# Performance work log

Measured on AMD Instinct MI355X. Metric: run time of the kernel, lower is better.

Reference implementation:

```python
import jax, jax.numpy as jnp
import numpy as np

N, E, B = 16384, 65536, 32
D_IN, ED, H, L = 4, 5, 64, 3  # node feat, edge feat, hidden=output, num layers
NEG_SLOPE = 0.1
EPS = 1e-5


def _leaky(v):
    return jnp.where(v > 0, v, NEG_SLOPE * v)


def setup_inputs() -> dict:
    key = jax.random.key(0)
    ks = jax.random.split(key, 32)
    s = 0.05
    inp = {
        'x': jax.random.normal(ks[0], (N, D_IN), jnp.float32),
        'edge_index': jax.random.randint(ks[1], (2, E), 0, N),
        'edge_attr': jax.random.normal(ks[2], (E, ED), jnp.float32),
        'batch': jnp.sort(jax.random.randint(ks[3], (N,), 0, B)),
        # input projection Linear(4 -> H)
        'W_in': s * jax.random.normal(ks[4], (H, D_IN), jnp.float32),
        'b_in': jnp.zeros((H,), jnp.float32),
        # per-layer edge MLP: Linear(ED->H), Linear(H->H), Linear(H->H*H); stacked over L
        'ew1': s * jax.random.normal(ks[5], (L, H, ED), jnp.float32),
        'eb1': jnp.zeros((L, H), jnp.float32),
        'ew2': s * jax.random.normal(ks[6], (L, H, H), jnp.float32),
        'eb2': jnp.zeros((L, H), jnp.float32),
        'ew3': s * jax.random.normal(ks[7], (L, H * H, H), jnp.float32),
        'eb3': jnp.zeros((L, H * H), jnp.float32),
        # NNConv root weight + bias per layer
        'root_w': s * jax.random.normal(ks[8], (L, H, H), jnp.float32),
        'root_b': jnp.zeros((L, H), jnp.float32),
        # LayerNorm per layer
        'ln_g': jnp.ones((L, H), jnp.float32),
        'ln_b': jnp.zeros((L, H), jnp.float32),
        # prediction head: Linear(H->H), Linear(H->H//2), Linear(H//2->1)
        'pw1': s * jax.random.normal(ks[9], (H, H), jnp.float32),
        'pb1': jnp.zeros((H,), jnp.float32),
        'pw2': s * jax.random.normal(ks[10], (H // 2, H), jnp.float32),
        'pb2': jnp.zeros((H // 2,), jnp.float32),
        'pw3': s * jax.random.normal(ks[11], (1, H // 2), jnp.float32),
        'pb3': jnp.zeros((1,), jnp.float32),
    }
    return inp


def reference(x, edge_index, edge_attr, batch, W_in, b_in, ew1, eb1, ew2, eb2,
              ew3, eb3, root_w, root_b, ln_g, ln_b, pw1, pb1, pw2, pb2, pw3, pb3):
    src, dst = edge_index[0], edge_index[1]
    n_nodes = x.shape[0]
    n_edges = edge_attr.shape[0]
    # in-degree for scatter-mean (PyG yields 0 for isolated nodes)
    deg = jax.ops.segment_sum(jnp.ones((n_edges,), x.dtype), dst, num_segments=n_nodes)
    deg = jnp.maximum(deg, 1.0)[:, None]

    # input projection (dropout = identity in eval)
    h = _leaky(x @ W_in.T + b_in)

    for l in range(L):
        # edge MLP -> per-edge weight matrix [E, H, H]
        e = _leaky(edge_attr @ ew1[l].T + eb1[l])
        e = _leaky(e @ ew2[l].T + eb2[l])
        Wf = (e @ ew3[l].T + eb3[l]).reshape(n_edges, H, H)
        # message = x_src @ W_edge, scatter-mean to dst
        msg = jnp.einsum('ei,eio->eo', h[src], Wf)
        agg = jax.ops.segment_sum(msg, dst, num_segments=n_nodes) / deg
        out = agg + h @ root_w[l].T + root_b[l]
        # LayerNorm (post-norm)
        mu = out.mean(-1, keepdims=True)
        var = ((out - mu) ** 2).mean(-1, keepdims=True)
        out = (out - mu) * jax.lax.rsqrt(var + EPS) * ln_g[l] + ln_b[l]
        # activation + (identity) dropout + residual (in==out for all layers)
        h = _leaky(out) + h

    # global mean pool over graphs
    pooled = jax.ops.segment_sum(h, batch, num_segments=B)
    cnt = jax.ops.segment_sum(jnp.ones((n_nodes,), h.dtype), batch, num_segments=B)
    pooled = pooled / jnp.maximum(cnt, 1.0)[:, None]

    # prediction head
    p = _leaky(pooled @ pw1.T + pb1)
    p = _leaky(p @ pw2.T + pb2)
    pred = (p @ pw3.T + pb3).squeeze(-1)  # [B]
    return pred
```

## Files before the change

kernel.cpp:

```cpp
#include <hip/hip_runtime.h>
#include <hip/hip_bf16.h>

#define N_NODES 16384
#define N_EDGES 65536
#define NB      32
#define H       64
#define NLAYERS 3
#define NEG     0.1f
#define LN_EPS  1e-5f

typedef _Float16 f16;
typedef _Float16 f16x2 __attribute__((ext_vector_type(2)));
typedef _Float16 f16x8 __attribute__((ext_vector_type(8)));
typedef __fp16   hf16x2 __attribute__((ext_vector_type(2)));
typedef float    f32x16 __attribute__((ext_vector_type(16)));

union F16x8 { f16x8 v; f16x2 p[4]; int4 i4; int2 i2[2]; };
union F16x2U { f16x2 h2; hf16x2 raw; unsigned int u; };
union F16U   { f16 h; unsigned short u; };

__device__ __forceinline__ f16x2 pkrtz(float a, float b) {
    F16x2U t; t.raw = __builtin_amdgcn_cvt_pkrtz(a, b); return t.h2;
}
__device__ __forceinline__ float leaky(float v) { return v > 0.f ? v : NEG * v; }

__global__ __launch_bounds__(256) void k_setup(const float* __restrict__ x,
                                               const float* __restrict__ Win,
                                               const float* __restrict__ bin,
                                               const int* __restrict__ dst,
                                               const float* __restrict__ ew3,
                                               const float* __restrict__ eb3,
                                               float* __restrict__ h,
                                               float* __restrict__ deg,
                                               f16* __restrict__ Bp) {
    int bid = blockIdx.x;
    if (bid < 4096) {
        int t = bid * 256 + threadIdx.x;
        int n = t >> 6, j = t & 63;
        const float* xr = x + n * 4;
        const float* wr = Win + j * 4;
        float v = bin[j] + xr[0] * wr[0] + xr[1] * wr[1] + xr[2] * wr[2] + xr[3] * wr[3];
        h[t] = leaky(v);
    } else if (bid < 4352) {
        int e = (bid - 4096) * 256 + threadIdx.x;
        atomicAdd(&deg[dst[e]], 1.0f);
    } else {
        int tg    = (bid - 4352) * 256 + threadIdx.x;
        int lane  = tg & 63;
        int gslot = tg >> 6;
        int l     = gslot / 520;
        int slot  = gslot - l * 520;
        const float* ew3l = ew3 + (size_t)l * 262144;
        const float* eb3l = eb3 + (size_t)l * 4096;
        int i   = slot >> 3;
        int rem = slot & 7;
        int ks  = rem >> 1;
        int oq  = rem & 1;
        int o   = oq * 32 + (lane & 31);
        int k0  = ks * 16 + (lane >> 5) * 8;
        float v[8];
        if (i < 64) {
            const float* s = ew3l + ((size_t)(i * 64 + o)) * 64 + k0;
            float4 a = ((const float4*)s)[0];
            float4 b = ((const float4*)s)[1];
            v[0] = a.x; v[1] = a.y; v[2] = a.z; v[3] = a.w;
            v[4] = b.x; v[5] = b.y; v[6] = b.z; v[7] = b.w;
        } else {
#pragma unroll
            for (int j = 0; j < 8; j++) v[j] = eb3l[(k0 + j) * 64 + o];
        }
        union { int4 i4; f16 a[8]; } out;
#pragma unroll
        for (int j = 0; j < 8; j++) out.a[j] = (f16)v[j];
        *(int4*)(Bp + (size_t)l * 266240 + (size_t)slot * 512 + lane * 8) = out.i4;
    }
}

#define HS_STRIDE 76

__device__ __forceinline__ void loadB8(const f16* __restrict__ Bp, int c, int oq, int lane, F16x8* dstB) {
    const f16* base = Bp + (((size_t)(c * 16 + oq)) << 9) + lane * 8;
#pragma unroll
    for (int di = 0; di < 2; di++)
#pragma unroll
        for (int ks = 0; ks < 4; ks++)
            dstB[di * 4 + ks].i4 = *(const int4*)(base + ((di * 8 + ks * 2) << 9));
}
__device__ __forceinline__ void loadB4(const f16* __restrict__ Bp, int oq, int lane, F16x8* dstB) {
    const f16* base = Bp + (((size_t)(512 + oq)) << 9) + lane * 8;
#pragma unroll
    for (int ks = 0; ks < 4; ks++)
        dstB[ks].i4 = *(const int4*)(base + ((ks * 2) << 9));
}

__device__ __forceinline__ void msg_chunk2(int c, const F16x8* __restrict__ B,
                                           const unsigned short* hp0,
                                           const unsigned short* hp1,
                                           const f16x2 (*e2p)[4][4], f32x16* CC) {
    unsigned int rr0 = *(const unsigned int*)(hp0 + 2 * c);
    unsigned int rr1 = *(const unsigned int*)(hp1 + 2 * c);
    F16x2U h00, h01, h10, h11;
    h00.u = __builtin_amdgcn_perm(rr0, rr0, 0x01000100u);
    h10.u = __builtin_amdgcn_perm(rr0, rr0, 0x03020302u);
    h01.u = __builtin_amdgcn_perm(rr1, rr1, 0x01000100u);
    h11.u = __builtin_amdgcn_perm(rr1, rr1, 0x03020302u);
#pragma unroll
    for (int ks = 0; ks < 4; ks++) {
        F16x8 A00, A01, A10, A11;
#pragma unroll
        for (int r = 0; r < 4; r++) {
            A00.p[r] = h00.h2 * e2p[0][ks][r];
            A01.p[r] = h01.h2 * e2p[1][ks][r];
            A10.p[r] = h10.h2 * e2p[0][ks][r];
            A11.p[r] = h11.h2 * e2p[1][ks][r];
        }
        CC[0] = __builtin_amdgcn_mfma_f32_32x32x16_f16(A00.v, B[0 * 4 + ks].v, CC[0], 0, 0, 0);
        CC[1] = __builtin_amdgcn_mfma_f32_32x32x16_f16(A01.v, B[0 * 4 + ks].v, CC[1], 0, 0, 0);
        CC[2] = __builtin_amdgcn_mfma_f32_32x32x16_f16(A10.v, B[1 * 4 + ks].v, CC[2], 0, 0, 0);
        CC[3] = __builtin_amdgcn_mfma_f32_32x32x16_f16(A11.v, B[1 * 4 + ks].v, CC[3], 0, 0, 0);
    }
}

__global__ __launch_bounds__(256, 2) void k_msg(const float* __restrict__ h,
                                                const float* __restrict__ ea,
                                                const float* __restrict__ w1,
                                                const float* __restrict__ b1,
                                                const float* __restrict__ w2,
                                                const float* __restrict__ b2,
                                                const f16* __restrict__ Bp,
                                                const int* __restrict__ src,
                                                const int* __restrict__ dst,
                                                float* __restrict__ agg) {
    __shared__ __align__(16) unsigned short hsL[128 * HS_STRIDE];
    __shared__ __align__(16) unsigned short e1L[128 * 72];
    __shared__ __align__(16) unsigned short e2L[128 * 72];
    __shared__ float eas[128 * 8];
    __shared__ int dstL[128];

    const int t    = threadIdx.x;
    const int lane = t & 63;
    const int w    = t >> 6;
    const int eh   = w >> 1, oq = w & 1;
    const int m    = lane & 31;
    const int kp   = lane >> 5;
    const int eb   = blockIdx.x * 128;

    for (int idx = t; idx < 640; idx += 256) {
        int r = idx / 5, d = idx - r * 5;
        eas[r * 8 + d] = ea[(size_t)eb * 5 + idx];
    }
    {
        int e    = t >> 1;
        int half = t & 1;
        int nsrc = src[eb + e];
        const float4* hr = (const float4*)(h + (size_t)nsrc * 64 + half * 32);
        unsigned int* hrow = (unsigned int*)hsL + e * (HS_STRIDE / 2) + half * 16;
#pragma unroll
        for (int q = 0; q < 8; q++) {
            float4 v = hr[q];
            F16x2U p0, p1;
            p0.raw = __builtin_amdgcn_cvt_pkrtz(v.x, v.y);
            p1.raw = __builtin_amdgcn_cvt_pkrtz(v.z, v.w);
            hrow[q * 2 + 0] = p0.u;
            hrow[q * 2 + 1] = p1.u;
        }
        if (t < 128) dstL[t] = dst[eb + t];
    }
    __syncthreads();

    {
        int kk = t & 63;
        int eg = t >> 6;
        float w1r[5];
#pragma unroll
        for (int d = 0; d < 5; d++) w1r[d] = w1[kk * 5 + d];
        float b1r = b1[kk];
#pragma unroll 4
        for (int g = 0; g < 32; g++) {
            int row = eg * 32 + g;
            float4 a4 = *(const float4*)(eas + row * 8);
            float a5 = eas[row * 8 + 4];
            float v = b1r + a4.x * w1r[0] + a4.y * w1r[1] + a4.z * w1r[2] + a4.w * w1r[3] + a5 * w1r[4];
            F16U z; z.h = (f16)leaky(v);
            e1L[row * 72 + kk] = z.u;
        }
    }
    __syncthreads();

    {
        F16x8 W2f[4];
#pragma unroll
        for (int ks = 0; ks < 4; ks++) {
            const float* s = w2 + (size_t)(oq * 32 + m) * 64 + ks * 16 + kp * 8;
            float4 a = ((const float4*)s)[0];
            float4 b = ((const float4*)s)[1];
            W2f[ks].p[0] = pkrtz(a.x, a.y);
            W2f[ks].p[1] = pkrtz(a.z, a.w);
            W2f[ks].p[2] = pkrtz(b.x, b.y);
            W2f[ks].p[3] = pkrtz(b.z, b.w);
        }
        float b2r = b2[oq * 32 + m];
#pragma unroll
        for (int tt = 0; tt < 2; tt++) {
            f32x16 C2 = {0,0,0,0,0,0,0,0,0,0,0,0,0,0,0,0};
#pragma unroll
            for (int ks = 0; ks < 4; ks++) {
                F16x8 A;
                A.i4 = *(const int4*)(e1L + (size_t)((eh * 2 + tt) * 32 + m) * 72 + ks * 16 + kp * 8);
                C2 = __builtin_amdgcn_mfma_f32_32x32x16_f16(A.v, W2f[ks].v, C2, 0, 0, 0);
            }
#pragma unroll
            for (int reg = 0; reg < 16; reg++) {
                int r = (reg & 3) + 8 * (reg >> 2) + 4 * kp;
                F16U z; z.h = (f16)leaky(C2[reg] + b2r);
                e2L[((eh * 2 + tt) * 32 + r) * 72 + oq * 32 + m] = z.u;
            }
        }
    }
    __syncthreads();

    f16x2 e2p[2][4][4];
#pragma unroll
    for (int tt = 0; tt < 2; tt++) {
#pragma unroll
        for (int ks = 0; ks < 4; ks++) {
            F16x8 q;
            q.i4 = *(const int4*)(e2L + (size_t)((eh * 2 + tt) * 32 + m) * 72 + ks * 16 + kp * 8);
            e2p[tt][ks][0] = q.p[0]; e2p[tt][ks][1] = q.p[1];
            e2p[tt][ks][2] = q.p[2]; e2p[tt][ks][3] = q.p[3];
        }
    }

    f32x16 CC[4];
#pragma unroll
    for (int q = 0; q < 4; q++)
#pragma unroll
        for (int r = 0; r < 16; r++) CC[q][r] = 0.f;

    const unsigned short* hp0 = hsL + ((eh * 2 + 0) * 32 + m) * HS_STRIDE;
    const unsigned short* hp1 = hsL + ((eh * 2 + 1) * 32 + m) * HS_STRIDE;

    F16x8 B0[8], B1[8];
    loadB8(Bp, 0, oq, lane, B0);
    loadB8(Bp, 1, oq, lane, B1);
    for (int it = 0; it < 15; it++) {
        int c = it * 2;
        msg_chunk2(c,     B0, hp0, hp1, e2p, CC);  loadB8(Bp, c + 2, oq, lane, B0);
        msg_chunk2(c + 1, B1, hp0, hp1, e2p, CC);  loadB8(Bp, c + 3, oq, lane, B1);
    }
    msg_chunk2(30, B0, hp0, hp1, e2p, CC);
    loadB4(Bp, oq, lane, B0);
    msg_chunk2(31, B1, hp0, hp1, e2p, CC);

#pragma unroll
    for (int ks = 0; ks < 4; ks++) {
        int koff = (ks * 16 + kp * 8) * 2;
        const char* r0p = (const char*)hsL + (size_t)((eh * 2 + 0) * 32 + m) * (HS_STRIDE * 2) + koff;
        const char* r1p = (const char*)hsL + (size_t)((eh * 2 + 1) * 32 + m) * (HS_STRIDE * 2) + koff;
        F16x8 A0, A1;
        A0.i2[0] = *(const int2*)(r0p); A0.i2[1] = *(const int2*)(r0p + 8);
        A1.i2[0] = *(const int2*)(r1p); A1.i2[1] = *(const int2*)(r1p + 8);
        CC[0] = __builtin_amdgcn_mfma_f32_32x32x16_f16(A0.v, B0[ks].v, CC[0], 0, 0, 0);
        CC[1] = __builtin_amdgcn_mfma_f32_32x32x16_f16(A1.v, B0[ks].v, CC[1], 0, 0, 0);
    }

    int o = oq * 32 + m;
#pragma unroll
    for (int reg = 0; reg < 16; reg++) {
        int r = (reg & 3) + 8 * (reg >> 2) + 4 * kp;
        atomicAdd(&agg[(size_t)dstL[(eh * 2 + 0) * 32 + r] * 64 + o], CC[0][reg] + CC[2][reg]);
    }
#pragma unroll
    for (int reg = 0; reg < 16; reg++) {
        int r = (reg & 3) + 8 * (reg >> 2) + 4 * kp;
        atomicAdd(&agg[(size_t)dstL[(eh * 2 + 1) * 32 + r] * 64 + o], CC[1][reg] + CC[3][reg]);
    }
}

__global__ __launch_bounds__(256) void k_node(const float* __restrict__ agg,
                                              const float* __restrict__ deg,
                                              const float* __restrict__ rw,
                                              const float* __restrict__ rb,
                                              const float* __restrict__ lg,
                                              const float* __restrict__ lb,
                                              float* __restrict__ h,
                                              const int* __restrict__ batch,
                                              float* __restrict__ pooled,
                                              int last) {
    __shared__ __align__(16) unsigned short hA[64 * 72];
    __shared__ float outL[64][68];
    int t = threadIdx.x;
    int nb = blockIdx.x * 64;
    int lane = t & 63, w = t >> 6;
    int nq = w >> 1, oq = w & 1;
    int m = lane & 31, kp = lane >> 5;

    {
        int r = t >> 2, c0 = (t & 3) * 16;
        const float4* hr = (const float4*)(h + (size_t)(nb + r) * 64 + c0);
        unsigned int* drow = (unsigned int*)hA + r * 36 + c0 / 2;
#pragma unroll
        for (int q = 0; q < 4; q++) {
            float4 v = hr[q];
            F16x2U p0, p1;
            p0.raw = __builtin_amdgcn_cvt_pkrtz(v.x, v.y);
            p1.raw = __builtin_amdgcn_cvt_pkrtz(v.z, v.w);
            drow[q * 2] = p0.u; drow[q * 2 + 1] = p1.u;
        }
    }
    F16x8 Bf[4];
#pragma unroll
    for (int ks = 0; ks < 4; ks++) {
        const float* s = rw + (size_t)(oq * 32 + m) * 64 + ks * 16 + kp * 8;
        float4 a = ((const float4*)s)[0];
        float4 b = ((const float4*)s)[1];
        Bf[ks].p[0] = pkrtz(a.x, a.y);
        Bf[ks].p[1] = pkrtz(a.z, a.w);
        Bf[ks].p[2] = pkrtz(b.x, b.y);
        Bf[ks].p[3] = pkrtz(b.z, b.w);
    }
    __syncthreads();

    f32x16 C = {0,0,0,0,0,0,0,0,0,0,0,0,0,0,0,0};
#pragma unroll
    for (int ks = 0; ks < 4; ks++) {
        F16x8 A;
        A.i4 = *(const int4*)(hA + (size_t)(nq * 32 + m) * 72 + ks * 16 + kp * 8);
        C = __builtin_amdgcn_mfma_f32_32x32x16_f16(A.v, Bf[ks].v, C, 0, 0, 0);
    }

    int o = oq * 32 + m;
#pragma unroll
    for (int reg = 0; reg < 16; reg++) {
        int r = (reg & 3) + 8 * (reg >> 2) + 4 * kp;
        int n = nq * 32 + r;
        outL[n][o] = C[reg] + rb[o] + agg[(size_t)(nb + n) * 64 + o] / fmaxf(deg[nb + n], 1.0f);
    }
    __syncthreads();

    float gj = lg[lane], bj = lb[lane];
    float accp = 0.f;
    int cur = batch[nb + w * 16];
    for (int q = 0; q < 16; q++) {
        int n = w * 16 + q;
        float v = outL[n][lane];
        float mu = v;
#pragma unroll
        for (int msk = 32; msk > 0; msk >>= 1) mu += __shfl_xor(mu, msk);
        mu *= (1.f / 64.f);
        float d = v - mu;
        float var = d * d;
#pragma unroll
        for (int msk = 32; msk > 0; msk >>= 1) var += __shfl_xor(var, msk);
        var *= (1.f / 64.f);
        float ov = d * rsqrtf(var + LN_EPS) * gj + bj;
        float hn = leaky(ov) + h[(size_t)(nb + n) * 64 + lane];
        h[(size_t)(nb + n) * 64 + lane] = hn;
        if (last) {
            int b = batch[nb + n];
            if (b != cur) { atomicAdd(&pooled[cur * 64 + lane], accp); accp = 0.f; cur = b; }
            accp += hn;
        }
    }
    if (last) atomicAdd(&pooled[cur * 64 + lane], accp);
}

__global__ __launch_bounds__(256) void k_head(const float* __restrict__ pooled,
                                              const int* __restrict__ batch,
                                              const float* __restrict__ pw1, const float* __restrict__ pb1,
                                              const float* __restrict__ pw2, const float* __restrict__ pb2,
                                              const float* __restrict__ pw3, const float* __restrict__ pb3,
                                              float* __restrict__ out) {
    __shared__ float cntL[32];
    __shared__ float ps[32][64];
    __shared__ float p1[32][64];
    __shared__ float p2[32][32];
    int t = threadIdx.x;
    if (t < 32) cntL[t] = 0.f;
    __syncthreads();
    {
        const int4* bp4 = (const int4*)(batch + t * 64);
        int cur = batch[t * 64];
        float c = 0.f;
        for (int q = 0; q < 16; q++) {
            int4 b4 = bp4[q];
            int bs[4] = { b4.x, b4.y, b4.z, b4.w };
#pragma unroll
            for (int e = 0; e < 4; e++) {
                if (bs[e] != cur) { atomicAdd(&cntL[cur], c); cur = bs[e]; c = 0.f; }
                c += 1.f;
            }
        }
        atomicAdd(&cntL[cur], c);
    }
    __syncthreads();
    for (int idx = t; idx < 2048; idx += 256) {
        int b = idx >> 6, j = idx & 63;
        ps[b][j] = pooled[idx] / fmaxf(cntL[b], 1.0f);
    }
    __syncthreads();
    for (int idx = t; idx < 2048; idx += 256) {
        int b = idx >> 6, j = idx & 63;
        float v = pb1[j];
#pragma unroll 8
        for (int i = 0; i < 64; i++) v += ps[b][i] * pw1[j * 64 + i];
        p1[b][j] = leaky(v);
    }
    __syncthreads();
    for (int idx = t; idx < 1024; idx += 256) {
        int b = idx >> 5, j = idx & 31;
        float v = pb2[j];
#pragma unroll 8
        for (int i = 0; i < 64; i++) v += p1[b][i] * pw2[j * 64 + i];
        p2[b][j] = leaky(v);
    }
    __syncthreads();
    if (t < 32) {
        float v = pb3[0];
#pragma unroll 8
        for (int i = 0; i < 32; i++) v += p2[t][i] * pw3[i];
        out[t] = v;
    }
}

extern "C" void kernel_launch(void* const* d_in, const int* in_sizes, int n_in,
                              void* d_out, int out_size, void* d_ws, size_t ws_size,
                              hipStream_t stream) {
    const float* x    = (const float*)d_in[0];
    const int*   eidx = (const int*)  d_in[1];
    const float* ea   = (const float*)d_in[2];
    const int*   bat  = (const int*)  d_in[3];
    const float* Win  = (const float*)d_in[4];
    const float* bin  = (const float*)d_in[5];
    const float* ew1  = (const float*)d_in[6];
    const float* eb1  = (const float*)d_in[7];
    const float* ew2  = (const float*)d_in[8];
    const float* eb2  = (const float*)d_in[9];
    const float* ew3  = (const float*)d_in[10];
    const float* eb3  = (const float*)d_in[11];
    const float* rw   = (const float*)d_in[12];
    const float* rb   = (const float*)d_in[13];
    const float* lg   = (const float*)d_in[14];
    const float* lb   = (const float*)d_in[15];
    const float* pw1  = (const float*)d_in[16];
    const float* pb1  = (const float*)d_in[17];
    const float* pw2  = (const float*)d_in[18];
    const float* pb2  = (const float*)d_in[19];
    const float* pw3  = (const float*)d_in[20];
    const float* pb3  = (const float*)d_in[21];
    float* out = (float*)d_out;

    float* ws     = (float*)d_ws;
    float* h      = ws;
    float* agg    = ws + 1048576;
    float* deg    = ws + 4194304;
    float* pooled = ws + 4210688;
    f16*   Bp     = (f16*)(ws + 4212800);

    const int* srcp = eidx;
    const int* dstp = eidx + N_EDGES;

    (void)hipMemsetAsync(agg, 0, (size_t)3164224 * sizeof(float), stream);

    k_setup<<<4742, 256, 0, stream>>>(x, Win, bin, dstp, ew3, eb3, h, deg, Bp);

    for (int l = 0; l < NLAYERS; l++) {
        float* agg_l = agg + (size_t)l * N_NODES * H;
        k_msg <<<N_EDGES / 128, 256, 0, stream>>>(h, ea, ew1 + l * 320, eb1 + l * 64,
                                                  ew2 + l * 4096, eb2 + l * 64,
                                                  Bp + (size_t)l * 266240,
                                                  srcp, dstp, agg_l);
        k_node<<<N_NODES / 64, 256, 0, stream>>>(agg_l, deg, rw + l * 4096, rb + l * 64,
                                                 lg + l * 64, lb + l * 64, h,
                                                 bat, pooled, l == NLAYERS - 1 ? 1 : 0);
    }

    k_head<<<1, 256, 0, stream>>>(pooled, bat, pw1, pb1, pw2, pb2, pw3, pb3, out);
}
```

Baseline: 325.6 us.

## Fuse all stages into one persistent cooperative kernel with grid syncs

Replaces the memset, setup, per-layer message/node kernels and head with a single cooperative launch of 256 blocks that uses grid.sync between stages. Each block processes two edge tiles per layer and one node tile, and shared memory is unioned across stages. The aim is to remove the roughly nine kernel launch gaps and the separate memset. In exchange it runs at one block per CU with 256 blocks, so occupancy and latency hiding during the heavy message phase may be lower than with the previous 512-block, two-blocks-per-CU launch. It falls back to the multi-kernel path if the cooperative launch fails.

```diff
diff --git a/kernel.cpp b/kernel.cpp
--- a/kernel.cpp
+++ b/kernel.cpp
@@ -1,5 +1,8 @@
 #include <hip/hip_runtime.h>
+#include <hip/hip_cooperative_groups.h>
 #include <hip/hip_bf16.h>
+
+namespace cg = cooperative_groups;
 
 #define N_NODES 16384
 #define N_EDGES 65536
@@ -8,6 +11,7 @@
 #define NLAYERS 3
 #define NEG     0.1f
 #define LN_EPS  1e-5f
+#define HS_STRIDE 76
 
 typedef _Float16 f16;
 typedef _Float16 f16x2 __attribute__((ext_vector_type(2)));
@@ -23,6 +27,444 @@
     F16x2U t; t.raw = __builtin_amdgcn_cvt_pkrtz(a, b); return t.h2;
 }
 __device__ __forceinline__ float leaky(float v) { return v > 0.f ? v : NEG * v; }
+
+struct Params {
+    const float* x; const int* eidx; const float* ea; const int* bat;
+    const float* Win; const float* bin;
+    const float* ew1; const float* eb1; const float* ew2; const float* eb2;
+    const float* ew3; const float* eb3;
+    const float* rw;  const float* rb;  const float* lg;  const float* lb;
+    const float* pw1; const float* pb1; const float* pw2; const float* pb2;
+    const float* pw3; const float* pb3;
+    float* out; float* ws;
+};
+
+struct MsgSmem {
+    unsigned short hsL[128 * HS_STRIDE];
+    unsigned short e1L[128 * 72];
+    unsigned short e2L[128 * 72];
+    float eas[128 * 8];
+    int dstL[128];
+};
+struct NodeSmem {
+    unsigned short hA[64 * 72];
+    float outL[64][68];
+};
+struct HeadSmem {
+    float cntL[32];
+    float ps[32][64];
+    float p1[32][64];
+    float p2[32][32];
+};
+union __align__(16) AllSmem { MsgSmem m; NodeSmem n; HeadSmem hd; };
+
+__device__ __forceinline__ void loadB8(const f16* __restrict__ Bp, int c, int oq, int lane, F16x8* dstB) {
+    const f16* base = Bp + (((size_t)(c * 16 + oq)) << 9) + lane * 8;
+#pragma unroll
+    for (int di = 0; di < 2; di++)
+#pragma unroll
+        for (int ks = 0; ks < 4; ks++)
+            dstB[di * 4 + ks].i4 = *(const int4*)(base + ((di * 8 + ks * 2) << 9));
+}
+__device__ __forceinline__ void loadB4(const f16* __restrict__ Bp, int oq, int lane, F16x8* dstB) {
+    const f16* base = Bp + (((size_t)(512 + oq)) << 9) + lane * 8;
+#pragma unroll
+    for (int ks = 0; ks < 4; ks++)
+        dstB[ks].i4 = *(const int4*)(base + ((ks * 2) << 9));
+}
+
+__device__ __forceinline__ void msg_chunk2(int c, const F16x8* __restrict__ B,
+                                           const unsigned short* hp0,
+                                           const unsigned short* hp1,
+                                           const f16x2 (*e2p)[4][4], f32x16* CC) {
+    unsigned int rr0 = *(const unsigned int*)(hp0 + 2 * c);
+    unsigned int rr1 = *(const unsigned int*)(hp1 + 2 * c);
+    F16x2U h00, h01, h10, h11;
+    h00.u = __builtin_amdgcn_perm(rr0, rr0, 0x01000100u);
+    h10.u = __builtin_amdgcn_perm(rr0, rr0, 0x03020302u);
+    h01.u = __builtin_amdgcn_perm(rr1, rr1, 0x01000100u);
+    h11.u = __builtin_amdgcn_perm(rr1, rr1, 0x03020302u);
+#pragma unroll
+    for (int ks = 0; ks < 4; ks++) {
+        F16x8 A00, A01, A10, A11;
+#pragma unroll
+        for (int r = 0; r < 4; r++) {
+            A00.p[r] = h00.h2 * e2p[0][ks][r];
+            A01.p[r] = h01.h2 * e2p[1][ks][r];
+            A10.p[r] = h10.h2 * e2p[0][ks][r];
+            A11.p[r] = h11.h2 * e2p[1][ks][r];
+        }
+        CC[0] = __builtin_amdgcn_mfma_f32_32x32x16_f16(A00.v, B[0 * 4 + ks].v, CC[0], 0, 0, 0);
+        CC[1] = __builtin_amdgcn_mfma_f32_32x32x16_f16(A01.v, B[0 * 4 + ks].v, CC[1], 0, 0, 0);
+        CC[2] = __builtin_amdgcn_mfma_f32_32x32x16_f16(A10.v, B[1 * 4 + ks].v, CC[2], 0, 0, 0);
+        CC[3] = __builtin_amdgcn_mfma_f32_32x32x16_f16(A11.v, B[1 * 4 + ks].v, CC[3], 0, 0, 0);
+    }
+}
+
+__device__ __forceinline__ void msg_body(MsgSmem& S, const float* __restrict__ h,
+        const float* __restrict__ ea,
+        const float* __restrict__ w1, const float* __restrict__ b1,
+        const float* __restrict__ w2, const float* __restrict__ b2,
+        const f16* __restrict__ Bpl,
+        const int* __restrict__ srcp, const int* __restrict__ dstp,
+        float* __restrict__ agg_l, int eb, int t) {
+    const int lane = t & 63;
+    const int w    = t >> 6;
+    const int eh   = w >> 1, oq = w & 1;
+    const int m    = lane & 31;
+    const int kp   = lane >> 5;
+
+    for (int idx = t; idx < 640; idx += 256) {
+        int r = idx / 5, d = idx - r * 5;
+        S.eas[r * 8 + d] = ea[(size_t)eb * 5 + idx];
+    }
+    {
+        int e    = t >> 1;
+        int half = t & 1;
+        int nsrc = srcp[eb + e];
+        const float4* hr = (const float4*)(h + (size_t)nsrc * 64 + half * 32);
+        unsigned int* hrow = (unsigned int*)S.hsL + e * (HS_STRIDE / 2) + half * 16;
+#pragma unroll
+        for (int q = 0; q < 8; q++) {
+            float4 v = hr[q];
+            F16x2U p0, p1;
+            p0.raw = __builtin_amdgcn_cvt_pkrtz(v.x, v.y);
+            p1.raw = __builtin_amdgcn_cvt_pkrtz(v.z, v.w);
+            hrow[q * 2 + 0] = p0.u;
+            hrow[q * 2 + 1] = p1.u;
+        }
+        if (t < 128) S.dstL[t] = dstp[eb + t];
+    }
+    __syncthreads();
+
+    {
+        int kk = t & 63;
+        int eg = t >> 6;
+        float w1r[5];
+#pragma unroll
+        for (int d = 0; d < 5; d++) w1r[d] = w1[kk * 5 + d];
+        float b1r = b1[kk];
+#pragma unroll 4
+        for (int g = 0; g < 32; g++) {
+            int row = eg * 32 + g;
+            float4 a4 = *(const float4*)(S.eas + row * 8);
+            float a5 = S.eas[row * 8 + 4];
+            float v = b1r + a4.x * w1r[0] + a4.y * w1r[1] + a4.z * w1r[2] + a4.w * w1r[3] + a5 * w1r[4];
+            F16U z; z.h = (f16)leaky(v);
+            S.e1L[row * 72 + kk] = z.u;
+        }
+    }
+    __syncthreads();
+
+    {
+        F16x8 W2f[4];
+#pragma unroll
+        for (int ks = 0; ks < 4; ks++) {
+            const float* s = w2 + (size_t)(oq * 32 + m) * 64 + ks * 16 + kp * 8;
+            float4 a = ((const float4*)s)[0];
+            float4 b = ((const float4*)s)[1];
+            W2f[ks].p[0] = pkrtz(a.x, a.y);
+            W2f[ks].p[1] = pkrtz(a.z, a.w);
+            W2f[ks].p[2] = pkrtz(b.x, b.y);
+            W2f[ks].p[3] = pkrtz(b.z, b.w);
+        }
+        float b2r = b2[oq * 32 + m];
+#pragma unroll
+        for (int tt = 0; tt < 2; tt++) {
+            f32x16 C2 = {0,0,0,0,0,0,0,0,0,0,0,0,0,0,0,0};
+#pragma unroll
+            for (int ks = 0; ks < 4; ks++) {
+                F16x8 A;
+                A.i4 = *(const int4*)(S.e1L + (size_t)((eh * 2 + tt) * 32 + m) * 72 + ks * 16 + kp * 8);
+                C2 = __builtin_amdgcn_mfma_f32_32x32x16_f16(A.v, W2f[ks].v, C2, 0, 0, 0);
+            }
+#pragma unroll
+            for (int reg = 0; reg < 16; reg++) {
+                int r = (reg & 3) + 8 * (reg >> 2) + 4 * kp;
+                F16U z; z.h = (f16)leaky(C2[reg] + b2r);
+                S.e2L[((eh * 2 + tt) * 32 + r) * 72 + oq * 32 + m] = z.u;
+            }
+        }
+    }
+    __syncthreads();
+
+    f16x2 e2p[2][4][4];
+#pragma unroll
+    for (int tt = 0; tt < 2; tt++) {
+#pragma unroll
+        for (int ks = 0; ks < 4; ks++) {
+            F16x8 q;
+            q.i4 = *(const int4*)(S.e2L + (size_t)((eh * 2 + tt) * 32 + m) * 72 + ks * 16 + kp * 8);
+            e2p[tt][ks][0] = q.p[0]; e2p[tt][ks][1] = q.p[1];
+            e2p[tt][ks][2] = q.p[2]; e2p[tt][ks][3] = q.p[3];
+        }
+    }
+
+    f32x16 CC[4];
+#pragma unroll
+    for (int q = 0; q < 4; q++)
+#pragma unroll
+        for (int r = 0; r < 16; r++) CC[q][r] = 0.f;
+
+    const unsigned short* hp0 = S.hsL + ((eh * 2 + 0) * 32 + m) * HS_STRIDE;
+    const unsigned short* hp1 = S.hsL + ((eh * 2 + 1) * 32 + m) * HS_STRIDE;
+
+    F16x8 B0[8], B1[8];
+    loadB8(Bpl, 0, oq, lane, B0);
+    loadB8(Bpl, 1, oq, lane, B1);
+    for (int it = 0; it < 15; it++) {
+        int c = it * 2;
+        msg_chunk2(c,     B0, hp0, hp1, e2p, CC);  loadB8(Bpl, c + 2, oq, lane, B0);
+        msg_chunk2(c + 1, B1, hp0, hp1, e2p, CC);  loadB8(Bpl, c + 3, oq, lane, B1);
+    }
+    msg_chunk2(30, B0, hp0, hp1, e2p, CC);
+    loadB4(Bpl, oq, lane, B0);
+    msg_chunk2(31, B1, hp0, hp1, e2p, CC);
+#pragma unroll
+    for (int ks = 0; ks < 4; ks++) {
+        int koff = (ks * 16 + kp * 8) * 2;
+        const char* r0p = (const char*)S.hsL + (size_t)((eh * 2 + 0) * 32 + m) * (HS_STRIDE * 2) + koff;
+        const char* r1p = (const char*)S.hsL + (size_t)((eh * 2 + 1) * 32 + m) * (HS_STRIDE * 2) + koff;
+        F16x8 A0, A1;
+        A0.i2[0] = *(const int2*)(r0p); A0.i2[1] = *(const int2*)(r0p + 8);
+        A1.i2[0] = *(const int2*)(r1p); A1.i2[1] = *(const int2*)(r1p + 8);
+        CC[0] = __builtin_amdgcn_mfma_f32_32x32x16_f16(A0.v, B0[ks].v, CC[0], 0, 0, 0);
+        CC[1] = __builtin_amdgcn_mfma_f32_32x32x16_f16(A1.v, B0[ks].v, CC[1], 0, 0, 0);
+    }
+
+    int o = oq * 32 + m;
+#pragma unroll
+    for (int reg = 0; reg < 16; reg++) {
+        int r = (reg & 3) + 8 * (reg >> 2) + 4 * kp;
+        atomicAdd(&agg_l[(size_t)S.dstL[(eh * 2 + 0) * 32 + r] * 64 + o], CC[0][reg] + CC[2][reg]);
+    }
+#pragma unroll
+    for (int reg = 0; reg < 16; reg++) {
+        int r = (reg & 3) + 8 * (reg >> 2) + 4 * kp;
+        atomicAdd(&agg_l[(size_t)S.dstL[(eh * 2 + 1) * 32 + r] * 64 + o], CC[1][reg] + CC[3][reg]);
+    }
+}
+
+__device__ __forceinline__ void node_body(NodeSmem& S, float* __restrict__ h,
+        const float* __restrict__ agg_l, const float* __restrict__ deg,
+        const float* __restrict__ rwl, const float* __restrict__ rbl,
+        const float* __restrict__ lgl, const float* __restrict__ lbl,
+        const int* __restrict__ bat, float* __restrict__ pooled,
+        int last, int nb, int t) {
+    const int lane = t & 63, w = t >> 6;
+    const int nq = w >> 1, oq = w & 1;
+    const int m = lane & 31, kp = lane >> 5;
+
+    {
+        int r = t >> 2, c0 = (t & 3) * 16;
+        const float4* hr = (const float4*)(h + (size_t)(nb + r) * 64 + c0);
+        unsigned int* drow = (unsigned int*)S.hA + r * 36 + c0 / 2;
+#pragma unroll
+        for (int q = 0; q < 4; q++) {
+            float4 v = hr[q];
+            F16x2U p0, p1;
+            p0.raw = __builtin_amdgcn_cvt_pkrtz(v.x, v.y);
+            p1.raw = __builtin_amdgcn_cvt_pkrtz(v.z, v.w);
+            drow[q * 2] = p0.u; drow[q * 2 + 1] = p1.u;
+        }
+    }
+    F16x8 Bf[4];
+#pragma unroll
+    for (int ks = 0; ks < 4; ks++) {
+        const float* s = rwl + (size_t)(oq * 32 + m) * 64 + ks * 16 + kp * 8;
+        float4 a = ((const float4*)s)[0];
+        float4 b = ((const float4*)s)[1];
+        Bf[ks].p[0] = pkrtz(a.x, a.y);
+        Bf[ks].p[1] = pkrtz(a.z, a.w);
+        Bf[ks].p[2] = pkrtz(b.x, b.y);
+        Bf[ks].p[3] = pkrtz(b.z, b.w);
+    }
+    __syncthreads();
+
+    f32x16 C = {0,0,0,0,0,0,0,0,0,0,0,0,0,0,0,0};
+#pragma unroll
+    for (int ks = 0; ks < 4; ks++) {
+        F16x8 A;
+        A.i4 = *(const int4*)(S.hA + (size_t)(nq * 32 + m) * 72 + ks * 16 + kp * 8);
+        C = __builtin_amdgcn_mfma_f32_32x32x16_f16(A.v, Bf[ks].v, C, 0, 0, 0);
+    }
+
+    int o = oq * 32 + m;
+#pragma unroll
+    for (int reg = 0; reg < 16; reg++) {
+        int r = (reg & 3) + 8 * (reg >> 2) + 4 * kp;
+        int n = nq * 32 + r;
+        S.outL[n][o] = C[reg] + rbl[o] + agg_l[(size_t)(nb + n) * 64 + o] / fmaxf(deg[nb + n], 1.0f);
+    }
+    __syncthreads();
+
+    float gj = lgl[lane], bj = lbl[lane];
+    float accp = 0.f;
+    int cur = bat[nb + w * 16];
+    for (int q = 0; q < 16; q++) {
+        int n = w * 16 + q;
+        float v = S.outL[n][lane];
+        float mu = v;
+#pragma unroll
+        for (int msk = 32; msk > 0; msk >>= 1) mu += __shfl_xor(mu, msk);
+        mu *= (1.f / 64.f);
+        float d = v - mu;
+        float var = d * d;
+#pragma unroll
+        for (int msk = 32; msk > 0; msk >>= 1) var += __shfl_xor(var, msk);
+        var *= (1.f / 64.f);
+        float ov = d * rsqrtf(var + LN_EPS) * gj + bj;
+        float hn = leaky(ov) + h[(size_t)(nb + n) * 64 + lane];
+        h[(size_t)(nb + n) * 64 + lane] = hn;
+        if (last) {
+            int b = bat[nb + n];
+            if (b != cur) { atomicAdd(&pooled[cur * 64 + lane], accp); accp = 0.f; cur = b; }
+            accp += hn;
+        }
+    }
+    if (last) atomicAdd(&pooled[cur * 64 + lane], accp);
+}
+
+__device__ __forceinline__ void head_body(HeadSmem& S, const float* __restrict__ pooled,
+        const int* __restrict__ bat,
+        const float* pw1, const float* pb1, const float* pw2, const float* pb2,
+        const float* pw3, const float* pb3, float* __restrict__ out, int t) {
+    if (t < 32) S.cntL[t] = 0.f;
+    __syncthreads();
+    {
+        const int4* bp4 = (const int4*)(bat + t * 64);
+        int cur = bat[t * 64];
+        float c = 0.f;
+        for (int q = 0; q < 16; q++) {
+            int4 b4 = bp4[q];
+            int bs[4] = { b4.x, b4.y, b4.z, b4.w };
+#pragma unroll
+            for (int e = 0; e < 4; e++) {
+                if (bs[e] != cur) { atomicAdd(&S.cntL[cur], c); cur = bs[e]; c = 0.f; }
+                c += 1.f;
+            }
+        }
+        atomicAdd(&S.cntL[cur], c);
+    }
+    __syncthreads();
+    for (int idx = t; idx < 2048; idx += 256) {
+        int b = idx >> 6, j = idx & 63;
+        S.ps[b][j] = pooled[idx] / fmaxf(S.cntL[b], 1.0f);
+    }
+    __syncthreads();
+    for (int idx = t; idx < 2048; idx += 256) {
+        int b = idx >> 6, j = idx & 63;
+        float v = pb1[j];
+#pragma unroll 8
+        for (int i = 0; i < 64; i++) v += S.ps[b][i] * pw1[j * 64 + i];
+        S.p1[b][j] = leaky(v);
+    }
+    __syncthreads();
+    for (int idx = t; idx < 1024; idx += 256) {
+        int b = idx >> 5, j = idx & 31;
+        float v = pb2[j];
+#pragma unroll 8
+        for (int i = 0; i < 64; i++) v += S.p1[b][i] * pw2[j * 64 + i];
+        S.p2[b][j] = leaky(v);
+    }
+    __syncthreads();
+    if (t < 32) {
+        float v = pb3[0];
+#pragma unroll 8
+        for (int i = 0; i < 32; i++) v += S.p2[t][i] * pw3[i];
+        out[t] = v;
+    }
+}
+
+__global__ __launch_bounds__(256, 1) void k_all(Params P) {
+    __shared__ AllSmem smem;
+    cg::grid_group grid = cg::this_grid();
+
+    const int t    = threadIdx.x;
+    const int bid  = blockIdx.x;
+    const int lane = t & 63;
+    const int w    = t >> 6;
+    const int m    = lane & 31;
+    const int kp   = lane >> 5;
+
+    float* ws     = P.ws;
+    float* h      = ws;
+    float* agg    = ws + 1048576;
+    float* deg    = ws + 4194304;
+    float* pooled = ws + 4210688;
+    f16*   Bp     = (f16*)(ws + 4212800);
+    const int* srcp = P.eidx;
+    const int* dstp = P.eidx + N_EDGES;
+
+    {
+        float4* z = (float4*)(ws + 1048576);
+        for (int i = bid * 256 + t; i < 791056; i += 256 * 256)
+            z[i] = make_float4(0.f, 0.f, 0.f, 0.f);
+    }
+    grid.sync();
+
+    {
+        int base = bid * 4096;
+#pragma unroll
+        for (int q = 0; q < 16; q++) {
+            int idx = base + q * 256 + t;
+            int n = idx >> 6, j = idx & 63;
+            const float* xr = P.x + n * 4;
+            const float* wr = P.Win + j * 4;
+            float v = P.bin[j] + xr[0] * wr[0] + xr[1] * wr[1] + xr[2] * wr[2] + xr[3] * wr[3];
+            h[idx] = leaky(v);
+        }
+        atomicAdd(&deg[dstp[bid * 256 + t]], 1.0f);
+        for (int gslot = bid * 4 + w; gslot < 1560; gslot += 1024) {
+            int l     = gslot / 520;
+            int slot  = gslot - l * 520;
+            const float* ew3l = P.ew3 + (size_t)l * 262144;
+            const float* eb3l = P.eb3 + (size_t)l * 4096;
+            int i   = slot >> 3;
+            int rem = slot & 7;
+            int ks  = rem >> 1;
+            int oq  = rem & 1;
+            int o   = oq * 32 + m;
+            int k0  = ks * 16 + kp * 8;
+            float v[8];
+            if (i < 64) {
+                const float* s = ew3l + ((size_t)(i * 64 + o)) * 64 + k0;
+                float4 a = ((const float4*)s)[0];
+                float4 b = ((const float4*)s)[1];
+                v[0] = a.x; v[1] = a.y; v[2] = a.z; v[3] = a.w;
+                v[4] = b.x; v[5] = b.y; v[6] = b.z; v[7] = b.w;
+            } else {
+#pragma unroll
+                for (int j = 0; j < 8; j++) v[j] = eb3l[(k0 + j) * 64 + o];
+            }
+            union { int4 i4; f16 a[8]; } outw;
+#pragma unroll
+            for (int j = 0; j < 8; j++) outw.a[j] = (f16)v[j];
+            *(int4*)(Bp + (size_t)l * 266240 + (size_t)slot * 512 + lane * 8) = outw.i4;
+        }
+    }
+    grid.sync();
+
+    for (int l = 0; l < NLAYERS; l++) {
+        float* agg_l = agg + (size_t)l * 1048576;
+#pragma unroll 1
+        for (int g = 0; g < 2; g++) {
+            if (g) __syncthreads();
+            msg_body(smem.m, h, P.ea, P.ew1 + l * 320, P.eb1 + l * 64,
+                     P.ew2 + l * 4096, P.eb2 + l * 64,
+                     Bp + (size_t)l * 266240, srcp, dstp, agg_l,
+                     (g * 256 + bid) * 128, t);
+        }
+        grid.sync();
+        node_body(smem.n, h, agg_l, deg, P.rw + l * 4096, P.rb + l * 64,
+                  P.lg + l * 64, P.lb + l * 64, P.bat, pooled,
+                  (l == NLAYERS - 1) ? 1 : 0, bid * 64, t);
+        grid.sync();
+    }
+
+    if (bid == 0)
+        head_body(smem.hd, pooled, P.bat, P.pw1, P.pb1, P.pw2, P.pb2, P.pw3, P.pb3, P.out, t);
+}
 
 __global__ __launch_bounds__(256) void k_setup(const float* __restrict__ x,
                                                const float* __restrict__ Win,
@@ -69,411 +511,105 @@
 #pragma unroll
             for (int j = 0; j < 8; j++) v[j] = eb3l[(k0 + j) * 64 + o];
         }
-        union { int4 i4; f16 a[8]; } out;
-#pragma unroll
-        for (int j = 0; j < 8; j++) out.a[j] = (f16)v[j];
-        *(int4*)(Bp + (size_t)l * 266240 + (size_t)slot * 512 + lane * 8) = out.i4;
-    }
-}
-
-#define HS_STRIDE 76
-
-__device__ __forceinline__ void loadB8(const f16* __restrict__ Bp, int c, int oq, int lane, F16x8* dstB) {
-    const f16* base = Bp + (((size_t)(c * 16 + oq)) << 9) + lane * 8;
-#pragma unroll
-    for (int di = 0; di < 2; di++)
-#pragma unroll
-        for (int ks = 0; ks < 4; ks++)
-            dstB[di * 4 + ks].i4 = *(const int4*)(base + ((di * 8 + ks * 2) << 9));
-}
-__device__ __forceinline__ void loadB4(const f16* __restrict__ Bp, int oq, int lane, F16x8* dstB) {
-    const f16* base = Bp + (((size_t)(512 + oq)) << 9) + lane * 8;
-#pragma unroll
-    for (int ks = 0; ks < 4; ks++)
-        dstB[ks].i4 = *(const int4*)(base + ((ks * 2) << 9));
-}
-
-__device__ __forceinline__ void msg_chunk2(int c, const F16x8* __restrict__ B,
-                                           const unsigned short* hp0,
-                                           const unsigned short* hp1,
-                                           const f16x2 (*e2p)[4][4], f32x16* CC) {
-    unsigned int rr0 = *(const unsigned int*)(hp0 + 2 * c);
-    unsigned int rr1 = *(const unsigned int*)(hp1 + 2 * c);
-    F16x2U h00, h01, h10, h11;
-    h00.u = __builtin_amdgcn_perm(rr0, rr0, 0x01000100u);
-    h10.u = __builtin_amdgcn_perm(rr0, rr0, 0x03020302u);
-    h01.u = __builtin_amdgcn_perm(rr1, rr1, 0x01000100u);
-    h11.u = __builtin_amdgcn_perm(rr1, rr1, 0x03020302u);
-#pragma unroll
-    for (int ks = 0; ks < 4; ks++) {
-        F16x8 A00, A01, A10, A11;
-#pragma unroll
-        for (int r = 0; r < 4; r++) {
-            A00.p[r] = h00.h2 * e2p[0][ks][r];
-            A01.p[r] = h01.h2 * e2p[1][ks][r];
-            A10.p[r] = h10.h2 * e2p[0][ks][r];
-            A11.p[r] = h11.h2 * e2p[1][ks][r];
-        }
-        CC[0] = __builtin_amdgcn_mfma_f32_32x32x16_f16(A00.v, B[0 * 4 + ks].v, CC[0], 0, 0, 0);
-        CC[1] = __builtin_amdgcn_mfma_f32_32x32x16_f16(A01.v, B[0 * 4 + ks].v, CC[1], 0, 0, 0);
-        CC[2] = __builtin_amdgcn_mfma_f32_32x32x16_f16(A10.v, B[1 * 4 + ks].v, CC[2], 0, 0, 0);
-        CC[3] = __builtin_amdgcn_mfma_f32_32x32x16_f16(A11.v, B[1 * 4 + ks].v, CC[3], 0, 0, 0);
-    }
-}
-
-__global__ __launch_bounds__(256, 2) void k_msg(const float* __restrict__ h,
-                                                const float* __restrict__ ea,
-                                                const float* __restrict__ w1,
-                                                const float* __restrict__ b1,
-                                                const float* __restrict__ w2,
-                                                const float* __restrict__ b2,
-                                                const f16* __restrict__ Bp,
-                                                const int* __restrict__ src,
-                                                const int* __restrict__ dst,
-                                                float* __restrict__ agg) {
-    __shared__ __align__(16) unsigned short hsL[128 * HS_STRIDE];
-    __shared__ __align__(16) unsigned short e1L[128 * 72];
-    __shared__ __align__(16) unsigned short e2L[128 * 72];
-    __shared__ float eas[128 * 8];
-    __shared__ int dstL[128];
-
-    const int t    = threadIdx.x;
-    const int lane = t & 63;
-    const int w    = t >> 6;
-    const int eh   = w >> 1, oq = w & 1;
-    const int m    = lane & 31;
-    const int kp   = lane >> 5;
-    const int eb   = blockIdx.x * 128;
-
-    for (int idx = t; idx < 640; idx += 256) {
-        int r = idx / 5, d = idx - r * 5;
-        eas[r * 8 + d] = ea[(size_t)eb * 5 + idx];
-    }
-    {
-        int e    = t >> 1;
-        int half = t & 1;
-        int nsrc = src[eb + e];
-        const float4* hr = (const float4*)(h + (size_t)nsrc * 64 + half * 32);
-        unsigned int* hrow = (unsigned int*)hsL + e * (HS_STRIDE / 2) + half * 16;
-#pragma unroll
-        for (int q = 0; q < 8; q++) {
-            float4 v = hr[q];
-            F16x2U p0, p1;
-            p0.raw = __builtin_amdgcn_cvt_pkrtz(v.x, v.y);
-            p1.raw = __builtin_amdgcn_cvt_pkrtz(v.z, v.w);
-            hrow[q * 2 + 0] = p0.u;
-            hrow[q * 2 + 1] = p1.u;
-        }
-        if (t < 128) dstL[t] = dst[eb + t];
-    }
-    __syncthreads();
-
-    {
-        int kk = t & 63;
-        int eg = t >> 6;
-        float w1r[5];
-#pragma unroll
-        for (int d = 0; d < 5; d++) w1r[d] = w1[kk * 5 + d];
-        float b1r = b1[kk];
-#pragma unroll 4
-        for (int g = 0; g < 32; g++) {
-            int row = eg * 32 + g;
-            float4 a4 = *(const float4*)(eas + row * 8);
-            float a5 = eas[row * 8 + 4];
-            float v = b1r + a4.x * w1r[0] + a4.y * w1r[1] + a4.z * w1r[2] + a4.w * w1r[3] + a5 * w1r[4];
-            F16U z; z.h = (f16)leaky(v);
-            e1L[row * 72 + kk] = z.u;
-        }
-    }
-    __syncthreads();
-
-    {
-        F16x8 W2f[4];
-#pragma unroll
-        for (int ks = 0; ks < 4; ks++) {
-            const float* s = w2 + (size_t)(oq * 32 + m) * 64 + ks * 16 + kp * 8;
-            float4 a = ((const float4*)s)[0];
-            float4 b = ((const float4*)s)[1];
-            W2f[ks].p[0] = pkrtz(a.x, a.y);
-            W2f[ks].p[1] = pkrtz(a.z, a.w);
-            W2f[ks].p[2] = pkrtz(b.x, b.y);
-            W2f[ks].p[3] = pkrtz(b.z, b.w);
-        }
-        float b2r = b2[oq * 32 + m];
-#pragma unroll
-        for (int tt = 0; tt < 2; tt++) {
-            f32x16 C2 = {0,0,0,0,0,0,0,0,0,0,0,0,0,0,0,0};
-#pragma unroll
-            for (int ks = 0; ks < 4; ks++) {
-                F16x8 A;
-                A.i4 = *(const int4*)(e1L + (size_t)((eh * 2 + tt) * 32 + m) * 72 + ks * 16 + kp * 8);
-                C2 = __builtin_amdgcn_mfma_f32_32x32x16_f16(A.v, W2f[ks].v, C2, 0, 0, 0);
-            }
-#pragma unroll
-            for (int reg = 0; reg < 16; reg++) {
-                int r = (reg & 3) + 8 * (reg >> 2) + 4 * kp;
-                F16U z; z.h = (f16)leaky(C2[reg] + b2r);
-                e2L[((eh * 2 + tt) * 32 + r) * 72 + oq * 32 + m] = z.u;
-            }
-        }
-    }
-    __syncthreads();
-
-    f16x2 e2p[2][4][4];
-#pragma unroll
-    for (int tt = 0; tt < 2; tt++) {
-#pragma unroll
-        for (int ks = 0; ks < 4; ks++) {
-            F16x8 q;
-            q.i4 = *(const int4*)(e2L + (size_t)((eh * 2 + tt) * 32 + m) * 72 + ks * 16 + kp * 8);
-            e2p[tt][ks][0] = q.p[0]; e2p[tt][ks][1] = q.p[1];
-            e2p[tt][ks][2] = q.p[2]; e2p[tt][ks][3] = q.p[3];
-        }
-    }
-
-    f32x16 CC[4];
-#pragma unroll
-    for (int q = 0; q < 4; q++)
-#pragma unroll
-        for (int r = 0; r < 16; r++) CC[q][r] = 0.f;
-
-    const unsigned short* hp0 = hsL + ((eh * 2 + 0) * 32 + m) * HS_STRIDE;
-    const unsigned short* hp1 = hsL + ((eh * 2 + 1) * 32 + m) * HS_STRIDE;
-
-    F16x8 B0[8], B1[8];
-    loadB8(Bp, 0, oq, lane, B0);
-    loadB8(Bp, 1, oq, lane, B1);
-    for (int it = 0; it < 15; it++) {
-        int c = it * 2;
-        msg_chunk2(c,     B0, hp0, hp1, e2p, CC);  loadB8(Bp, c + 2, oq, lane, B0);
-        msg_chunk2(c + 1, B1, hp0, hp1, e2p, CC);  loadB8(Bp, c + 3, oq, lane, B1);
-    }
-    msg_chunk2(30, B0, hp0, hp1, e2p, CC);
-    loadB4(Bp, oq, lane, B0);
-    msg_chunk2(31, B1, hp0, hp1, e2p, CC);
-
-#pragma unroll
-    for (int ks = 0; ks < 4; ks++) {
-        int koff = (ks * 16 + kp * 8) * 2;
-        const char* r0p = (const char*)hsL + (size_t)((eh * 2 + 0) * 32 + m) * (HS_STRIDE * 2) + koff;
-        const char* r1p = (const char*)hsL + (size_t)((eh * 2 + 1) * 32 + m) * (HS_STRIDE * 2) + koff;
-        F16x8 A0, A1;
-        A0.i2[0] = *(const int2*)(r0p); A0.i2[1] = *(const int2*)(r0p + 8);
-        A1.i2[0] = *(const int2*)(r1p); A1.i2[1] = *(const int2*)(r1p + 8);
-        CC[0] = __builtin_amdgcn_mfma_f32_32x32x16_f16(A0.v, B0[ks].v, CC[0], 0, 0, 0);
-        CC[1] = __builtin_amdgcn_mfma_f32_32x32x16_f16(A1.v, B0[ks].v, CC[1], 0, 0, 0);
-    }
-
-    int o = oq * 32 + m;
-#pragma unroll
-    for (int reg = 0; reg < 16; reg++) {
-        int r = (reg & 3) + 8 * (reg >> 2) + 4 * kp;
-        atomicAdd(&agg[(size_t)dstL[(eh * 2 + 0) * 32 + r] * 64 + o], CC[0][reg] + CC[2][reg]);
-    }
-#pragma unroll
-    for (int reg = 0; reg < 16; reg++) {
-        int r = (reg & 3) + 8 * (reg >> 2) + 4 * kp;
-        atomicAdd(&agg[(size_t)dstL[(eh * 2 + 1) * 32 + r] * 64 + o], CC[1][reg] + CC[3][reg]);
-    }
-}
-
-__global__ __launch_bounds__(256) void k_node(const float* __restrict__ agg,
-                                              const float* __restrict__ deg,
-                                              const float* __restrict__ rw,
-                                              const float* __restrict__ rb,
-                                              const float* __restrict__ lg,
-                                              const float* __restrict__ lb,
-                                              float* __restrict__ h,
-                                              const int* __restrict__ batch,
-                                              float* __restrict__ pooled,
-                                              int last) {
-    __shared__ __align__(16) unsigned short hA[64 * 72];
-    __shared__ float outL[64][68];
-    int t = threadIdx.x;
-    int nb = blockIdx.x * 64;
-    int lane = t & 63, w = t >> 6;
-    int nq = w >> 1, oq = w & 1;
-    int m = lane & 31, kp = lane >> 5;
-
-    {
-        int r = t >> 2, c0 = (t & 3) * 16;
-        const float4* hr = (const float4*)(h + (size_t)(nb + r) * 64 + c0);
-        unsigned int* drow = (unsigned int*)hA + r * 36 + c0 / 2;
-#pragma unroll
-        for (int q = 0; q < 4; q++) {
-            float4 v = hr[q];
-            F16x2U p0, p1;
-            p0.raw = __builtin_amdgcn_cvt_pkrtz(v.x, v.y);
-            p1.raw = __builtin_amdgcn_cvt_pkrtz(v.z, v.w);
-            drow[q * 2] = p0.u; drow[q * 2 + 1] = p1.u;
-        }
-    }
-    F16x8 Bf[4];
-#pragma unroll
-    for (int ks = 0; ks < 4; ks++) {
-        const float* s = rw + (size_t)(oq * 32 + m) * 64 + ks * 16 + kp * 8;
-        float4 a = ((const float4*)s)[0];
-        float4 b = ((const float4*)s)[1];
-        Bf[ks].p[0] = pkrtz(a.x, a.y);
-        Bf[ks].p[1] = pkrtz(a.z, a.w);
-        Bf[ks].p[2] = pkrtz(b.x, b.y);
-        Bf[ks].p[3] = pkrtz(b.z, b.w);
-    }
-    __syncthreads();
-
-    f32x16 C = {0,0,0,0,0,0,0,0,0,0,0,0,0,0,0,0};
-#pragma unroll
-    for (int ks = 0; ks < 4; ks++) {
-        F16x8 A;
-        A.i4 = *(const int4*)(hA + (size_t)(nq * 32 + m) * 72 + ks * 16 + kp * 8);
-        C = __builtin_amdgcn_mfma_f32_32x32x16_f16(A.v, Bf[ks].v, C, 0, 0, 0);
-    }
-
-    int o = oq * 32 + m;
-#pragma unroll
-    for (int reg = 0; reg < 16; reg++) {
-        int r = (reg & 3) + 8 * (reg >> 2) + 4 * kp;
-        int n = nq * 32 + r;
-        outL[n][o] = C[reg] + rb[o] + agg[(size_t)(nb + n) * 64 + o] / fmaxf(deg[nb + n], 1.0f);
-    }
-    __syncthreads();
-
-    float gj = lg[lane], bj = lb[lane];
-    float accp = 0.f;
-    int cur = batch[nb + w * 16];
-    for (int q = 0; q < 16; q++) {
-        int n = w * 16 + q;
-        float v = outL[n][lane];
-        float mu = v;
-#pragma unroll
-        for (int msk = 32; msk > 0; msk >>= 1) mu += __shfl_xor(mu, msk);
-        mu *= (1.f / 64.f);
-        float d = v - mu;
-        float var = d * d;
-#pragma unroll
-        for (int msk = 32; msk > 0; msk >>= 1) var += __shfl_xor(var, msk);
-        var *= (1.f / 64.f);
-        float ov = d * rsqrtf(var + LN_EPS) * gj + bj;
-        float hn = leaky(ov) + h[(size_t)(nb + n) * 64 + lane];
-        h[(size_t)(nb + n) * 64 + lane] = hn;
-        if (last) {
-            int b = batch[nb + n];
-            if (b != cur) { atomicAdd(&pooled[cur * 64 + lane], accp); accp = 0.f; cur = b; }
-            accp += hn;
-        }
-    }
-    if (last) atomicAdd(&pooled[cur * 64 + lane], accp);
-}
-
-__global__ __launch_bounds__(256) void k_head(const float* __restrict__ pooled,
-                                              const int* __restrict__ batch,
-                                              const float* __restrict__ pw1, const float* __restrict__ pb1,
-                                              const float* __restrict__ pw2, const float* __restrict__ pb2,
-                                              const float* __restrict__ pw3, const float* __restrict__ pb3,
-                                              float* __restrict__ out) {
-    __shared__ float cntL[32];
-    __shared__ float ps[32][64];
-    __shared__ float p1[32][64];
-    __shared__ float p2[32][32];
-    int t = threadIdx.x;
-    if (t < 32) cntL[t] = 0.f;
-    __syncthreads();
-    {
-        const int4* bp4 = (const int4*)(batch + t * 64);
-        int cur = batch[t * 64];
-        float c = 0.f;
-        for (int q = 0; q < 16; q++) {
-            int4 b4 = bp4[q];
-            int bs[4] = { b4.x, b4.y, b4.z, b4.w };
-#pragma unroll
-            for (int e = 0; e < 4; e++) {
-                if (bs[e] != cur) { atomicAdd(&cntL[cur], c); cur = bs[e]; c = 0.f; }
-                c += 1.f;
-            }
-        }
-        atomicAdd(&cntL[cur], c);
-    }
-    __syncthreads();
-    for (int idx = t; idx < 2048; idx += 256) {
-        int b = idx >> 6, j = idx & 63;
-        ps[b][j] = pooled[idx] / fmaxf(cntL[b], 1.0f);
-    }
-    __syncthreads();
-    for (int idx = t; idx < 2048; idx += 256) {
-        int b = idx >> 6, j = idx & 63;
-        float v = pb1[j];
-#pragma unroll 8
-        for (int i = 0; i < 64; i++) v += ps[b][i] * pw1[j * 64 + i];
-        p1[b][j] = leaky(v);
-    }
-    __syncthreads();
-    for (int idx = t; idx < 1024; idx += 256) {
-        int b = idx >> 5, j = idx & 31;
-        float v = pb2[j];
-#pragma unroll 8
-        for (int i = 0; i < 64; i++) v += p1[b][i] * pw2[j * 64 + i];
-        p2[b][j] = leaky(v);
-    }
-    __syncthreads();
-    if (t < 32) {
-        float v = pb3[0];
-#pragma unroll 8
-        for (int i = 0; i < 32; i++) v += p2[t][i] * pw3[i];
-        out[t] = v;
-    }
+        union { int4 i4; f16 a[8]; } outw;
+#pragma unroll
+        for (int j = 0; j < 8; j++) outw.a[j] = (f16)v[j];
+        *(int4*)(Bp + (size_t)l * 266240 + (size_t)slot * 512 + lane * 8) = outw.i4;
+    }
+}
+
+__global__ __launch_bounds__(256, 2) void k_msg_s(const float* __restrict__ h,
+                                                  const float* __restrict__ ea,
+                                                  const float* __restrict__ w1,
+                                                  const float* __restrict__ b1,
+                                                  const float* __restrict__ w2,
+                                                  const float* __restrict__ b2,
+                                                  const f16* __restrict__ Bp,
+                                                  const int* __restrict__ src,
+                                                  const int* __restrict__ dst,
+                                                  float* __restrict__ agg) {
+    __shared__ MsgSmem S;
+    msg_body(S, h, ea, w1, b1, w2, b2, Bp, src, dst, agg, blockIdx.x * 128, threadIdx.x);
+}
+
+__global__ __launch_bounds__(256) void k_node_s(const float* __restrict__ agg,
+                                                const float* __restrict__ deg,
+                                                const float* __restrict__ rw,
+                                                const float* __restrict__ rb,
+                                                const float* __restrict__ lg,
+                                                const float* __restrict__ lb,
+                                                float* __restrict__ h,
+                                                const int* __restrict__ batch,
+                                                float* __restrict__ pooled,
+                                                int last) {
+    __shared__ NodeSmem S;
+    node_body(S, h, agg, deg, rw, rb, lg, lb, batch, pooled, last, blockIdx.x * 64, threadIdx.x);
+}
+
+__global__ __launch_bounds__(256) void k_head_s(const float* __restrict__ pooled,
+                                                const int* __restrict__ batch,
+                                                const float* __restrict__ pw1, const float* __restrict__ pb1,
+                                                const float* __restrict__ pw2, const float* __restrict__ pb2,
+                                                const float* __restrict__ pw3, const float* __restrict__ pb3,
+                                                float* __restrict__ out) {
+    __shared__ HeadSmem S;
+    head_body(S, pooled, batch, pw1, pb1, pw2, pb2, pw3, pb3, out, threadIdx.x);
 }
 
 extern "C" void kernel_launch(void* const* d_in, const int* in_sizes, int n_in,
                               void* d_out, int out_size, void* d_ws, size_t ws_size,
                               hipStream_t stream) {
-    const float* x    = (const float*)d_in[0];
-    const int*   eidx = (const int*)  d_in[1];
-    const float* ea   = (const float*)d_in[2];
-    const int*   bat  = (const int*)  d_in[3];
-    const float* Win  = (const float*)d_in[4];
-    const float* bin  = (const float*)d_in[5];
-    const float* ew1  = (const float*)d_in[6];
-    const float* eb1  = (const float*)d_in[7];
-    const float* ew2  = (const float*)d_in[8];
-    const float* eb2  = (const float*)d_in[9];
-    const float* ew3  = (const float*)d_in[10];
-    const float* eb3  = (const float*)d_in[11];
-    const float* rw   = (const float*)d_in[12];
-    const float* rb   = (const float*)d_in[13];
-    const float* lg   = (const float*)d_in[14];
-    const float* lb   = (const float*)d_in[15];
-    const float* pw1  = (const float*)d_in[16];
-    const float* pb1  = (const float*)d_in[17];
-    const float* pw2  = (const float*)d_in[18];
-    const float* pb2  = (const float*)d_in[19];
-    const float* pw3  = (const float*)d_in[20];
-    const float* pb3  = (const float*)d_in[21];
-    float* out = (float*)d_out;
-
-    float* ws     = (float*)d_ws;
-    float* h      = ws;
-    float* agg    = ws + 1048576;
-    float* deg    = ws + 4194304;
-    float* pooled = ws + 4210688;
-    f16*   Bp     = (f16*)(ws + 4212800);
-
-    const int* srcp = eidx;
-    const int* dstp = eidx + N_EDGES;
-
-    (void)hipMemsetAsync(agg, 0, (size_t)3164224 * sizeof(float), stream);
-
-    k_setup<<<4742, 256, 0, stream>>>(x, Win, bin, dstp, ew3, eb3, h, deg, Bp);
-
-    for (int l = 0; l < NLAYERS; l++) {
-        float* agg_l = agg + (size_t)l * N_NODES * H;
-        k_msg <<<N_EDGES / 128, 256, 0, stream>>>(h, ea, ew1 + l * 320, eb1 + l * 64,
-                                                  ew2 + l * 4096, eb2 + l * 64,
-                                                  Bp + (size_t)l * 266240,
-                                                  srcp, dstp, agg_l);
-        k_node<<<N_NODES / 64, 256, 0, stream>>>(agg_l, deg, rw + l * 4096, rb + l * 64,
-                                                 lg + l * 64, lb + l * 64, h,
-                                                 bat, pooled, l == NLAYERS - 1 ? 1 : 0);
-    }
-
-    k_head<<<1, 256, 0, stream>>>(pooled, bat, pw1, pb1, pw2, pb2, pw3, pb3, out);
-}
+    Params hp;
+    hp.x    = (const float*)d_in[0];
+    hp.eidx = (const int*)  d_in[1];
+    hp.ea   = (const float*)d_in[2];
+    hp.bat  = (const int*)  d_in[3];
+    hp.Win  = (const float*)d_in[4];
+    hp.bin  = (const float*)d_in[5];
+    hp.ew1  = (const float*)d_in[6];
+    hp.eb1  = (const float*)d_in[7];
+    hp.ew2  = (const float*)d_in[8];
+    hp.eb2  = (const float*)d_in[9];
+    hp.ew3  = (const float*)d_in[10];
+    hp.eb3  = (const float*)d_in[11];
+    hp.rw   = (const float*)d_in[12];
+    hp.rb   = (const float*)d_in[13];
+    hp.lg   = (const float*)d_in[14];
+    hp.lb   = (const float*)d_in[15];
+    hp.pw1  = (const float*)d_in[16];
+    hp.pb1  = (const float*)d_in[17];
+    hp.pw2  = (const float*)d_in[18];
+    hp.pb2  = (const float*)d_in[19];
+    hp.pw3  = (const float*)d_in[20];
+    hp.pb3  = (const float*)d_in[21];
+    hp.out  = (float*)d_out;
+    hp.ws   = (float*)d_ws;
+
+    void* args[] = { (void*)&hp };
+    hipError_t err = hipLaunchCooperativeKernel(reinterpret_cast<void*>(k_all),
+                                                dim3(256), dim3(256), args, 0, stream);
+    if (err != hipSuccess) {
+        float* ws     = (float*)d_ws;
+        float* h      = ws;
+        float* agg    = ws + 1048576;
+        float* deg    = ws + 4194304;
+        float* pooled = ws + 4210688;
+        f16*   Bp     = (f16*)(ws + 4212800);
+        const int* srcp = (const int*)d_in[1];
+        const int* dstp = srcp + N_EDGES;
+
+        (void)hipMemsetAsync(agg, 0, (size_t)3164224 * sizeof(float), stream);
+        k_setup<<<4742, 256, 0, stream>>>(hp.x, hp.Win, hp.bin, dstp, hp.ew3, hp.eb3, h, deg, Bp);
+        for (int l = 0; l < NLAYERS; l++) {
+            float* agg_l = agg + (size_t)l * 1048576;
+            k_msg_s <<<N_EDGES / 128, 256, 0, stream>>>(h, hp.ea, hp.ew1 + l * 320, hp.eb1 + l * 64,
+                                                        hp.ew2 + l * 4096, hp.eb2 + l * 64,
+                                                        Bp + (size_t)l * 266240, srcp, dstp, agg_l);
+            k_node_s<<<N_NODES / 64, 256, 0, stream>>>(agg_l, deg, hp.rw + l * 4096, hp.rb + l * 64,
+                                                       hp.lg + l * 64, hp.lb + l * 64, h,
+                                                       hp.bat, pooled, l == NLAYERS - 1 ? 1 : 0);
+        }
+        k_head_s<<<1, 256, 0, stream>>>(pooled, hp.bat, hp.pw1, hp.pb1, hp.pw2, hp.pb2,
+                                        hp.pw3, hp.pb3, (float*)d_out);
+    }
+}
```

After: 614.0 us. 1.89x slower.
